# Performance work log

Measured on AMD Instinct MI355X. Metric: run time of the kernel, lower is better.

The kernel has to match this reference:

```python
import jax, jax.numpy as jnp
import numpy as np

N_S, N_T = 64, 32
N_EFF = N_S * N_T          # 2048
K_T1, K_T2 = 8, 8
BATCH = 16


def _orthonormal(key, n):
    q, _ = jnp.linalg.qr(jax.random.normal(key, (n, n), dtype=jnp.float32))
    return q.astype(jnp.float32)


def setup_inputs() -> dict:
    key = jax.random.key(0)
    ks = jax.random.split(key, 6)
    return {
        "s_effective_batch": jax.random.normal(ks[0], (BATCH, N_EFF), dtype=jnp.float32),
        "U_G": _orthonormal(ks[1], N_S),
        "U_P_T": _orthonormal(ks[2], N_T),
        "h0": jax.random.normal(ks[3], (N_EFF,), dtype=jnp.float32) * 0.01,
        "h_hat_1_coeffs": jax.random.normal(ks[4], (N_S, K_T1), dtype=jnp.float32) * 0.01,
        "H_hat_2_S": jax.random.normal(ks[5], (N_S, N_S), dtype=jnp.float32) * 0.01,
        "H_hat_2_T_coeffs": jax.random.normal(jax.random.fold_in(key, 7), (K_T2, K_T2), dtype=jnp.float32) * 0.01,
    }


def reference(s_effective_batch, U_G, U_P_T, h0, h_hat_1_coeffs, H_hat_2_S, H_hat_2_T_coeffs):
    # spatio-temporal basis via Kronecker product: [N_eff, N_eff]
    U_ST = jnp.kron(U_G, U_P_T)

    # GFT as in the module: s_hat = s @ U_ST
    s_hat = s_effective_batch @ U_ST                       # [B, N_eff]

    # linear (first-order Volterra) term
    Ub1 = U_P_T[:, :K_T1]                                  # [N_T, K1]
    full_h_hat_1 = (h_hat_1_coeffs @ Ub1.T).reshape(-1)    # [N_eff]
    z1 = (full_h_hat_1[None, :] * s_hat) @ U_ST            # iGFT as in module: @ U_ST

    # quadratic kernel H2 = kron(H2_S, Ub2 @ C @ Ub2^T)
    Ub2 = U_P_T[:, :K_T2]
    full_H2_T = Ub2 @ (H_hat_2_T_coeffs @ Ub2.T)           # [N_T, N_T]
    H2 = jnp.kron(H_hat_2_S, full_H2_T)                    # [N_eff, N_eff]

    # z2[b,i] = diag( U_ST (H2 * s_hat_b s_hat_b^T) U_ST^T )_i
    #         = sum_{k,l} B[b,i,k] H2[k,l] B[b,i,l], with B[b,i,k] = U_ST[i,k]*s_hat[b,k]
    B = U_ST[None, :, :] * s_hat[:, None, :]               # [B, N_eff, N_eff]
    z2 = jnp.einsum('bik,kl,bil->bi', B, H2, B)            # batched GEMM + row-reduce

    return h0[None, :] + z1 + z2
```

## Files before the change

kernel.cpp:

```cpp
#include <hip/hip_runtime.h>


typedef short  bf16x8 __attribute__((ext_vector_type(8)));
typedef float  f32x4  __attribute__((ext_vector_type(4)));
typedef unsigned short u16;

static __device__ __forceinline__ u16 f2bf(float f) {
  unsigned u = __float_as_uint(f);
  u = (u + 0x7fff + ((u >> 16) & 1)) >> 16;
  return (u16)u;
}
static __device__ __forceinline__ float bf2f(u16 h) {
  return __uint_as_float(((unsigned)h) << 16);
}
static __device__ __forceinline__ float dot4(f32x4 a, f32x4 b) {
  return a.x * b.x + a.y * b.y + a.z * b.z + a.w * b.w;
}

__global__ __launch_bounds__(512) void volterra_one(
    const float* __restrict__ s, const float* __restrict__ UG,
    const float* __restrict__ UPT, const float* __restrict__ h0,
    const float* __restrict__ h1c, const float* __restrict__ HS,
    const float* __restrict__ Hc, float* __restrict__ out)
{
  const int b   = blockIdx.x >> 4;
  const int iT0 = (blockIdx.x & 15) << 1;
  const int t   = threadIdx.x;
  const int w   = t >> 6;
  const int l   = t & 63;
  const int r   = l & 15;
  const int g   = l >> 4;

  __shared__ __align__(16) float sS[64][36];
  __shared__ __align__(16) float sT1[64][36];
  __shared__ __align__(16) u16   sUGh[4096];
  __shared__ __align__(16) u16   sUPTTh[32 * 40];
  __shared__ __align__(16) u16   sUPTTl[32 * 40];
  __shared__ __align__(16) float sUPT[32][36];
  __shared__ __align__(16) float sHS[64][68];
  __shared__ float sUhc[32 * 9];
  __shared__ __align__(16) float wGm[2][8 * 36], wA[2][8 * 36], wQ[2][8 * 36];
  __shared__ __align__(16) float sGm[2][64][12], sA[2][64][12];
  __shared__ __align__(16) u16   sE[2][4096];
  __shared__ float wv[2][64];
  __shared__ float zp1[2][4][64];
  __shared__ float zpart[2][4][64];

  {
    const f32x4 v = ((const f32x4*)(s + b * 2048))[t];
    *(f32x4*)&sS[t >> 3][(t & 7) * 4] = v;
  }
  #pragma unroll
  for (int o4 = t, it = 0; it < 2; ++it, o4 += 512) {
    const int rr = o4 >> 4, c0 = (o4 & 15) * 4;
    const f32x4 v = ((const f32x4*)UG)[o4];
    short4 h;
    h.x = (short)f2bf(v.x); h.y = (short)f2bf(v.y);
    h.z = (short)f2bf(v.z); h.w = (short)f2bf(v.w);
    *(short4*)&sUGh[rr * 64 + (c0 ^ ((rr & 7) << 3))] = h;
  }
  #pragma unroll
  for (int o4 = t, it = 0; it < 2; ++it, o4 += 512) {
    const int rr = o4 >> 4, c0 = (o4 & 15) * 4;
    *(f32x4*)&sHS[rr][c0] = ((const f32x4*)HS)[o4];
  }
  if (t < 256) {
    const int k = t >> 3, c4 = t & 7;
    const f32x4 v = ((const f32x4*)UPT)[t];
    *(f32x4*)&sUPT[k][c4 * 4] = v;
    float arr[4] = {v.x, v.y, v.z, v.w};
    #pragma unroll
    for (int i = 0; i < 4; ++i) {
      const int c = 4 * c4 + i;
      const u16 hi = f2bf(arr[i]);
      sUPTTh[c * 40 + k] = hi;
      sUPTTl[c * 40 + k] = f2bf(arr[i] - bf2f(hi));
    }
    const int p = t & 7;
    float a = 0.f;
    #pragma unroll
    for (int q = 0; q < 8; ++q) a += UPT[k * 32 + q] * Hc[q * 8 + p];
    sUhc[k * 9 + p] = a;
  }
  __syncthreads();

  {
    const int side = t >> 8, p = (t >> 5) & 7, k = t & 31;
    const int iTs = iT0 + side;
    const float m1 = sUPT[iTs][k];
    const float m3 = sUPT[k][iTs];
    const float m2 = sUPT[k][p];
    wGm[side][p * 36 + k] = m1 * m2;
    wA [side][p * 36 + k] = m1 * sUhc[k * 9 + p];
    wQ [side][p * 36 + k] = m3 * m2;
  }
  {
    const int band = w >> 1, ct = w & 1;
    f32x4 acc = {0.f, 0.f, 0.f, 0.f};
    #pragma unroll
    for (int kc = 0; kc < 2; ++kc) {
      float av[8], bv[8];
      #pragma unroll
      for (int j = 0; j < 8; ++j)
        av[j] = UG[(kc * 32 + g * 8 + j) * 64 + 16 * band + r];
      #pragma unroll
      for (int j = 0; j < 8; ++j)
        bv[j] = sS[kc * 32 + g * 8 + j][ct * 16 + r];
      bf16x8 Ah, Al, Bh, Bl;
      #pragma unroll
      for (int j = 0; j < 8; ++j) {
        u16 h = f2bf(av[j]);
        Ah[j] = (short)h; Al[j] = (short)f2bf(av[j] - bf2f(h));
        h = f2bf(bv[j]);
        Bh[j] = (short)h; Bl[j] = (short)f2bf(bv[j] - bf2f(h));
      }
      acc = __builtin_amdgcn_mfma_f32_16x16x32_bf16(Ah, Bh, acc, 0, 0, 0);
      acc = __builtin_amdgcn_mfma_f32_16x16x32_bf16(Ah, Bl, acc, 0, 0, 0);
      acc = __builtin_amdgcn_mfma_f32_16x16x32_bf16(Al, Bh, acc, 0, 0, 0);
    }
    #pragma unroll
    for (int reg = 0; reg < 4; ++reg)
      sT1[16 * band + 4 * g + reg][ct * 16 + r] = acc[reg];
  }
  __syncthreads();

  {
    const int band = w >> 1, ct = w & 1;
    const f32x4 a0 = *(const f32x4*)&sT1[16 * band + r][g * 8];
    const f32x4 a1 = *(const f32x4*)&sT1[16 * band + r][g * 8 + 4];
    float av[8] = {a0.x, a0.y, a0.z, a0.w, a1.x, a1.y, a1.z, a1.w};
    bf16x8 Ah, Al;
    #pragma unroll
    for (int j = 0; j < 8; ++j) {
      const u16 h = f2bf(av[j]);
      Ah[j] = (short)h; Al[j] = (short)f2bf(av[j] - bf2f(h));
    }
    const bf16x8 Bh = *(const bf16x8*)&sUPTTh[(ct * 16 + r) * 40 + g * 8];
    const bf16x8 Bl = *(const bf16x8*)&sUPTTl[(ct * 16 + r) * 40 + g * 8];
    f32x4 acc = {0.f, 0.f, 0.f, 0.f};
    acc = __builtin_amdgcn_mfma_f32_16x16x32_bf16(Ah, Bh, acc, 0, 0, 0);
    acc = __builtin_amdgcn_mfma_f32_16x16x32_bf16(Ah, Bl, acc, 0, 0, 0);
    acc = __builtin_amdgcn_mfma_f32_16x16x32_bf16(Al, Bh, acc, 0, 0, 0);
    #pragma unroll
    for (int reg = 0; reg < 4; ++reg)
      sS[16 * band + 4 * g + reg][ct * 16 + r] = acc[reg];
  }
  __syncthreads();

  {
    const int side = t >> 8, ts = t & 255;
    const int kSa = ts >> 3, p = ts & 7;
    float g0 = 0.f, g1v = 0.f, a0 = 0.f, a1v = 0.f, q0 = 0.f, q1v = 0.f;
    #pragma unroll
    for (int c4 = 0; c4 < 8; ++c4) {
      const f32x4 w1 = *(const f32x4*)&wGm[side][p * 36 + c4 * 4];
      const f32x4 w2 = *(const f32x4*)&wA [side][p * 36 + c4 * 4];
      const f32x4 w3 = *(const f32x4*)&wQ [side][p * 36 + c4 * 4];
      const f32x4 x0 = *(const f32x4*)&sS[kSa][c4 * 4];
      const f32x4 x1 = *(const f32x4*)&sS[kSa + 32][c4 * 4];
      g0  += dot4(x0, w1); a0  += dot4(x0, w2); q0  += dot4(x0, w3);
      g1v += dot4(x1, w1); a1v += dot4(x1, w2); q1v += dot4(x1, w3);
    }
    sGm[side][kSa][p] = g0; sGm[side][kSa + 32][p] = g1v;
    sA [side][kSa][p] = a0; sA [side][kSa + 32][p] = a1v;
    float wv0 = h1c[kSa * 8 + p] * q0;
    float wv1 = h1c[(kSa + 32) * 8 + p] * q1v;
    wv0 += __shfl_xor(wv0, 1); wv0 += __shfl_xor(wv0, 2); wv0 += __shfl_xor(wv0, 4);
    wv1 += __shfl_xor(wv1, 1); wv1 += __shfl_xor(wv1, 2); wv1 += __shfl_xor(wv1, 4);
    if (p == 0) { wv[side][kSa] = wv0; wv[side][kSa + 32] = wv1; }
  }
  __syncthreads();

  {
    const int side = t >> 8, sub = (t >> 6) & 3;
    const f32x4 gr0 = *(const f32x4*)&sGm[side][l][0];
    const f32x4 gr1 = *(const f32x4*)&sGm[side][l][4];
    #pragma unroll 4
    for (int j = 0; j < 16; ++j) {
      const int kS = 4 * j + sub;
      const f32x4 a0v = *(const f32x4*)&sA[side][kS][0];
      const f32x4 a1v = *(const f32x4*)&sA[side][kS][4];
      const float e = (dot4(a0v, gr0) + dot4(a1v, gr1)) * sHS[kS][l];
      sE[side][kS * 64 + (l ^ ((kS & 7) << 3))] = f2bf(e);
    }
    const float wvl = wv[side][l];
    float part = 0.f;
    #pragma unroll
    for (int j = 0; j < 16; ++j) {
      const int kk = 16 * sub + j;
      part += __shfl(wvl, kk) * UG[kk * 64 + l];
    }
    zp1[side][sub][l] = part;
  }
  __syncthreads();

  {
    const int side = t >> 8, sub = (t >> 6) & 3;
    f32x4 acc[4];
    #pragma unroll
    for (int nt = 0; nt < 4; ++nt) acc[nt] = (f32x4){0.f, 0.f, 0.f, 0.f};
    #pragma unroll
    for (int ks = 0; ks < 2; ++ks) {
      const int kcol = g * 8 + ks * 32;
      const int rowA = 16 * sub + r;
      const bf16x8 ah = *(const bf16x8*)&sE[side][rowA * 64 + (kcol ^ ((rowA & 7) << 3))];
      #pragma unroll
      for (int nt = 0; nt < 4; ++nt) {
        const int rowB = 16 * nt + r;
        const bf16x8 bh = *(const bf16x8*)&sUGh[rowB * 64 + (kcol ^ ((rowB & 7) << 3))];
        acc[nt] = __builtin_amdgcn_mfma_f32_16x16x32_bf16(ah, bh, acc[nt], 0, 0, 0);
      }
    }
    #pragma unroll
    for (int nt = 0; nt < 4; ++nt) {
      float zp = 0.f;
      #pragma unroll
      for (int reg = 0; reg < 4; ++reg) {
        const int kS = 16 * sub + 4 * g + reg;
        const int iS = 16 * nt + r;
        zp += bf2f(sUGh[iS * 64 + (kS ^ ((iS & 7) << 3))]) * acc[nt][reg];
      }
      zp += __shfl_xor(zp, 16);
      zp += __shfl_xor(zp, 32);
      if (g == 0) zpart[side][sub][16 * nt + r] = zp;
    }
  }
  __syncthreads();

  if (t < 128) {
    const int side = t >> 6, c = t & 63;
    const float z2 = zpart[side][0][c] + zpart[side][1][c] +
                     zpart[side][2][c] + zpart[side][3][c];
    const float z1 = zp1[side][0][c] + zp1[side][1][c] +
                     zp1[side][2][c] + zp1[side][3][c];
    const int col = c * 32 + iT0 + side;
    out[b * 2048 + col] = h0[col] + z1 + z2;
  }
}

extern "C" void kernel_launch(void* const* d_in, const int* in_sizes, int n_in,
                              void* d_out, int out_size, void* d_ws, size_t ws_size,
                              hipStream_t stream) {
  const float* s   = (const float*)d_in[0];
  const float* UG  = (const float*)d_in[1];
  const float* UPT = (const float*)d_in[2];
  const float* h0  = (const float*)d_in[3];
  const float* h1c = (const float*)d_in[4];
  const float* HS  = (const float*)d_in[5];
  const float* Hc  = (const float*)d_in[6];
  float* out = (float*)d_out;

  volterra_one<<<256, 512, 0, stream>>>(s, UG, UPT, h0, h1c, HS, Hc, out);
}
```

Measured before the change: 15.04 us.

## Fold temporal GFT into weight vectors and stage split-bf16 operands in LDS

Removes the second MFMA stage, which multiplied by U_P_T. It does this by pre-multiplying the small temporal weight vectors (Gm, A, Q) by U_P_T in a scalar fp32 stage, so the spatial GEMM result feeds the reductions directly. The s and U_G operands are pre-split into hi/lo bf16 and written transposed and swizzled into LDS at load time, so the MFMA loop reads bf16x8 vectors instead of doing strided global loads and per-element conversions. This drops one block-wide barrier and the conversion work. In exchange it adds LDS footprint and scalar-heavy global reads of UPT and Hc in the weight setup.

```diff
diff --git a/kernel.cpp b/kernel.cpp
--- a/kernel.cpp
+++ b/kernel.cpp
@@ -31,89 +31,87 @@
   const int r   = l & 15;
   const int g   = l >> 4;
 
-  __shared__ __align__(16) float sS[64][36];
-  __shared__ __align__(16) float sT1[64][36];
+  __shared__ __align__(16) u16   sSTh[2048], sSTl[2048];
+  __shared__ __align__(16) u16   sUGTh[4096], sUGTl[4096];
   __shared__ __align__(16) u16   sUGh[4096];
-  __shared__ __align__(16) u16   sUPTTh[32 * 40];
-  __shared__ __align__(16) u16   sUPTTl[32 * 40];
   __shared__ __align__(16) float sUPT[32][36];
   __shared__ __align__(16) float sHS[64][68];
-  __shared__ float sUhc[32 * 9];
-  __shared__ __align__(16) float wGm[2][8 * 36], wA[2][8 * 36], wQ[2][8 * 36];
+  __shared__ __align__(16) float wGmR[2][288], wAR[2][288], wQR[2][288];
+  __shared__ __align__(16) float wGmP[2][288], wAP[2][288], wQP[2][288];
+  __shared__ __align__(16) float sT1[64][36];
   __shared__ __align__(16) float sGm[2][64][12], sA[2][64][12];
   __shared__ __align__(16) u16   sE[2][4096];
   __shared__ float wv[2][64];
-  __shared__ float zp1[2][4][64];
-  __shared__ float zpart[2][4][64];
+  __shared__ float zp1[2][4][64], zpart[2][4][64];
 
   {
     const f32x4 v = ((const f32x4*)(s + b * 2048))[t];
-    *(f32x4*)&sS[t >> 3][(t & 7) * 4] = v;
+    const int rr = t >> 3, c0 = (t & 7) * 4;
+    const float arr[4] = {v.x, v.y, v.z, v.w};
+    #pragma unroll
+    for (int i = 0; i < 4; ++i) {
+      const int c = c0 + i;
+      const u16 hi = f2bf(arr[i]);
+      const int ad = c * 64 + (((rr >> 3) ^ (c & 7)) << 3) + (rr & 7);
+      sSTh[ad] = hi;
+      sSTl[ad] = f2bf(arr[i] - bf2f(hi));
+    }
   }
   #pragma unroll
-  for (int o4 = t, it = 0; it < 2; ++it, o4 += 512) {
+  for (int it = 0; it < 2; ++it) {
+    const int o4 = t + it * 512;
     const int rr = o4 >> 4, c0 = (o4 & 15) * 4;
     const f32x4 v = ((const f32x4*)UG)[o4];
-    short4 h;
-    h.x = (short)f2bf(v.x); h.y = (short)f2bf(v.y);
-    h.z = (short)f2bf(v.z); h.w = (short)f2bf(v.w);
-    *(short4*)&sUGh[rr * 64 + (c0 ^ ((rr & 7) << 3))] = h;
+    const float arr[4] = {v.x, v.y, v.z, v.w};
+    short4 h4;
+    h4.x = (short)f2bf(v.x); h4.y = (short)f2bf(v.y);
+    h4.z = (short)f2bf(v.z); h4.w = (short)f2bf(v.w);
+    *(short4*)&sUGh[rr * 64 + (c0 ^ ((rr & 7) << 3))] = h4;
+    #pragma unroll
+    for (int i = 0; i < 4; ++i) {
+      const int c = c0 + i;
+      const u16 hi = f2bf(arr[i]);
+      const int ad = c * 64 + (((rr >> 3) ^ (c & 7)) << 3) + (rr & 7);
+      sUGTh[ad] = hi;
+      sUGTl[ad] = f2bf(arr[i] - bf2f(hi));
+    }
   }
   #pragma unroll
-  for (int o4 = t, it = 0; it < 2; ++it, o4 += 512) {
-    const int rr = o4 >> 4, c0 = (o4 & 15) * 4;
-    *(f32x4*)&sHS[rr][c0] = ((const f32x4*)HS)[o4];
+  for (int it = 0; it < 2; ++it) {
+    const int o4 = t + it * 512;
+    *(f32x4*)&sHS[o4 >> 4][(o4 & 15) * 4] = ((const f32x4*)HS)[o4];
   }
   if (t < 256) {
-    const int k = t >> 3, c4 = t & 7;
-    const f32x4 v = ((const f32x4*)UPT)[t];
-    *(f32x4*)&sUPT[k][c4 * 4] = v;
-    float arr[4] = {v.x, v.y, v.z, v.w};
-    #pragma unroll
-    for (int i = 0; i < 4; ++i) {
-      const int c = 4 * c4 + i;
-      const u16 hi = f2bf(arr[i]);
-      sUPTTh[c * 40 + k] = hi;
-      sUPTTl[c * 40 + k] = f2bf(arr[i] - bf2f(hi));
-    }
-    const int p = t & 7;
-    float a = 0.f;
-    #pragma unroll
-    for (int q = 0; q < 8; ++q) a += UPT[k * 32 + q] * Hc[q * 8 + p];
-    sUhc[k * 9 + p] = a;
-  }
-  __syncthreads();
-
+    *(f32x4*)&sUPT[t >> 3][(t & 7) * 4] = ((const f32x4*)UPT)[t];
+  }
   {
     const int side = t >> 8, p = (t >> 5) & 7, k = t & 31;
     const int iTs = iT0 + side;
-    const float m1 = sUPT[iTs][k];
-    const float m3 = sUPT[k][iTs];
-    const float m2 = sUPT[k][p];
-    wGm[side][p * 36 + k] = m1 * m2;
-    wA [side][p * 36 + k] = m1 * sUhc[k * 9 + p];
-    wQ [side][p * 36 + k] = m3 * m2;
-  }
+    const float m1 = UPT[iTs * 32 + k];
+    const float m3 = UPT[k * 32 + iTs];
+    const float m2 = UPT[k * 32 + p];
+    float uh = 0.f;
+    #pragma unroll
+    for (int q = 0; q < 8; ++q) uh += UPT[k * 32 + q] * Hc[q * 8 + p];
+    wGmR[side][p * 36 + k] = m1 * m2;
+    wAR [side][p * 36 + k] = m1 * uh;
+    wQR [side][p * 36 + k] = m3 * m2;
+  }
+  __syncthreads();
+
   {
     const int band = w >> 1, ct = w & 1;
+    const int rowA = 16 * band + r, rowB = ct * 16 + r;
     f32x4 acc = {0.f, 0.f, 0.f, 0.f};
     #pragma unroll
     for (int kc = 0; kc < 2; ++kc) {
-      float av[8], bv[8];
-      #pragma unroll
-      for (int j = 0; j < 8; ++j)
-        av[j] = UG[(kc * 32 + g * 8 + j) * 64 + 16 * band + r];
-      #pragma unroll
-      for (int j = 0; j < 8; ++j)
-        bv[j] = sS[kc * 32 + g * 8 + j][ct * 16 + r];
-      bf16x8 Ah, Al, Bh, Bl;
-      #pragma unroll
-      for (int j = 0; j < 8; ++j) {
-        u16 h = f2bf(av[j]);
-        Ah[j] = (short)h; Al[j] = (short)f2bf(av[j] - bf2f(h));
-        h = f2bf(bv[j]);
-        Bh[j] = (short)h; Bl[j] = (short)f2bf(bv[j] - bf2f(h));
-      }
+      const int ch = kc * 4 + g;
+      const int oa = rowA * 64 + ((ch ^ (rowA & 7)) << 3);
+      const int ob = rowB * 64 + ((ch ^ (rowB & 7)) << 3);
+      const bf16x8 Ah = *(const bf16x8*)&sUGTh[oa];
+      const bf16x8 Al = *(const bf16x8*)&sUGTl[oa];
+      const bf16x8 Bh = *(const bf16x8*)&sSTh[ob];
+      const bf16x8 Bl = *(const bf16x8*)&sSTl[ob];
       acc = __builtin_amdgcn_mfma_f32_16x16x32_bf16(Ah, Bh, acc, 0, 0, 0);
       acc = __builtin_amdgcn_mfma_f32_16x16x32_bf16(Ah, Bl, acc, 0, 0, 0);
       acc = __builtin_amdgcn_mfma_f32_16x16x32_bf16(Al, Bh, acc, 0, 0, 0);
@@ -122,28 +120,20 @@
     for (int reg = 0; reg < 4; ++reg)
       sT1[16 * band + 4 * g + reg][ct * 16 + r] = acc[reg];
   }
-  __syncthreads();
-
-  {
-    const int band = w >> 1, ct = w & 1;
-    const f32x4 a0 = *(const f32x4*)&sT1[16 * band + r][g * 8];
-    const f32x4 a1 = *(const f32x4*)&sT1[16 * band + r][g * 8 + 4];
-    float av[8] = {a0.x, a0.y, a0.z, a0.w, a1.x, a1.y, a1.z, a1.w};
-    bf16x8 Ah, Al;
-    #pragma unroll
-    for (int j = 0; j < 8; ++j) {
-      const u16 h = f2bf(av[j]);
-      Ah[j] = (short)h; Al[j] = (short)f2bf(av[j] - bf2f(h));
-    }
-    const bf16x8 Bh = *(const bf16x8*)&sUPTTh[(ct * 16 + r) * 40 + g * 8];
-    const bf16x8 Bl = *(const bf16x8*)&sUPTTl[(ct * 16 + r) * 40 + g * 8];
-    f32x4 acc = {0.f, 0.f, 0.f, 0.f};
-    acc = __builtin_amdgcn_mfma_f32_16x16x32_bf16(Ah, Bh, acc, 0, 0, 0);
-    acc = __builtin_amdgcn_mfma_f32_16x16x32_bf16(Ah, Bl, acc, 0, 0, 0);
-    acc = __builtin_amdgcn_mfma_f32_16x16x32_bf16(Al, Bh, acc, 0, 0, 0);
-    #pragma unroll
-    for (int reg = 0; reg < 4; ++reg)
-      sS[16 * band + 4 * g + reg][ct * 16 + r] = acc[reg];
+  {
+    const int side = t >> 8, p = (t >> 5) & 7, j = t & 31;
+    float aG = 0.f, aA = 0.f, aQ = 0.f;
+    #pragma unroll
+    for (int k4 = 0; k4 < 8; ++k4) {
+      const f32x4 u  = *(const f32x4*)&sUPT[j][k4 * 4];
+      const f32x4 w1 = *(const f32x4*)&wGmR[side][p * 36 + k4 * 4];
+      const f32x4 w2 = *(const f32x4*)&wAR [side][p * 36 + k4 * 4];
+      const f32x4 w3 = *(const f32x4*)&wQR [side][p * 36 + k4 * 4];
+      aG += dot4(u, w1); aA += dot4(u, w2); aQ += dot4(u, w3);
+    }
+    wGmP[side][p * 36 + j] = aG;
+    wAP [side][p * 36 + j] = aA;
+    wQP [side][p * 36 + j] = aQ;
   }
   __syncthreads();
 
@@ -153,11 +143,11 @@
     float g0 = 0.f, g1v = 0.f, a0 = 0.f, a1v = 0.f, q0 = 0.f, q1v = 0.f;
     #pragma unroll
     for (int c4 = 0; c4 < 8; ++c4) {
-      const f32x4 w1 = *(const f32x4*)&wGm[side][p * 36 + c4 * 4];
-      const f32x4 w2 = *(const f32x4*)&wA [side][p * 36 + c4 * 4];
-      const f32x4 w3 = *(const f32x4*)&wQ [side][p * 36 + c4 * 4];
-      const f32x4 x0 = *(const f32x4*)&sS[kSa][c4 * 4];
-      const f32x4 x1 = *(const f32x4*)&sS[kSa + 32][c4 * 4];
+      const f32x4 w1 = *(const f32x4*)&wGmP[side][p * 36 + c4 * 4];
+      const f32x4 w2 = *(const f32x4*)&wAP [side][p * 36 + c4 * 4];
+      const f32x4 w3 = *(const f32x4*)&wQP [side][p * 36 + c4 * 4];
+      const f32x4 x0 = *(const f32x4*)&sT1[kSa][c4 * 4];
+      const f32x4 x1 = *(const f32x4*)&sT1[kSa + 32][c4 * 4];
       g0  += dot4(x0, w1); a0  += dot4(x0, w2); q0  += dot4(x0, w3);
       g1v += dot4(x1, w1); a1v += dot4(x1, w2); q1v += dot4(x1, w3);
     }
```

Result: faster. 13.71 us (-8.8%).
